# Kernel tuning notes

Hardware: AMD Instinct MI355X
Metric: run time of the kernel (lower is better)

The kernel has to match this reference:

```python
import jax, jax.numpy as jnp
import numpy as np

N, E, G = 100000, 400000, 2000   # nodes, edges, graphs
IN, H = 48, 128                  # in_channels, hidden_channels (= out_channels)
L = 6                            # num GIN layers
EPS = 1e-5                       # BatchNorm eps
SLOPE = 0.01                     # leaky_relu negative slope


def setup_inputs() -> dict:
    key = jax.random.key(0)
    ks = jax.random.split(key, 12)
    x = jax.random.normal(ks[0], (N, IN), jnp.float32)
    edge_index = jax.random.randint(ks[1], (2, E), 0, N)
    edge_attr = jax.random.normal(ks[2], (E, 4), jnp.float32)  # ignored by GINConv
    # sorted graph-assignment vector; guarantee every graph has >=1 node
    batch = jnp.sort(jnp.concatenate([jnp.arange(G),
                                      jax.random.randint(ks[3], (N - G,), 0, G)]))
    s = 0.05
    W1a = jax.random.normal(ks[4], (IN, H), jnp.float32) * s        # layer-0 MLP lin1
    W1b = jax.random.normal(ks[5], (L - 1, H, H), jnp.float32) * s  # layers 1..5 MLP lin1
    b1 = jnp.zeros((L, H), jnp.float32)
    g1 = jnp.ones((L, H), jnp.float32)    # inner BN scale
    be1 = jnp.zeros((L, H), jnp.float32)  # inner BN bias
    W2 = jax.random.normal(ks[6], (L, H, H), jnp.float32) * s       # MLP lin2
    b2 = jnp.zeros((L, H), jnp.float32)
    gn = jnp.ones((L - 1, H), jnp.float32)    # outer BN scale (layers 0..4)
    bn_b = jnp.zeros((L - 1, H), jnp.float32) # outer BN bias
    fc_w = jax.random.normal(ks[7], (2 * H, 64), jnp.float32) * s
    fc_b = jnp.zeros((64,), jnp.float32)
    fc2_w = jax.random.normal(ks[8], (64, 3), jnp.float32) * s
    fc2_b = jnp.zeros((3,), jnp.float32)
    return dict(x=x, edge_attr=edge_attr, W1a=W1a, W1b=W1b, b1=b1, g1=g1, be1=be1,
                W2=W2, b2=b2, gn=gn, bn_b=bn_b, fc_w=fc_w, fc_b=fc_b,
                fc2_w=fc2_w, fc2_b=fc2_b, edge_index=edge_index, batch=batch,
                num_graphs=G)


def _bn(h, g, b):
    # training-mode BatchNorm1d over node dim (biased variance, as torch)
    m = jnp.mean(h, axis=0)
    v = jnp.mean((h - m) ** 2, axis=0)
    return g * (h - m) * jax.lax.rsqrt(v + EPS) + b


def _lrelu(h):
    return jnp.where(h >= 0, h, SLOPE * h)


def reference(x, edge_attr, W1a, W1b, b1, g1, be1, W2, b2, gn, bn_b,
              fc_w, fc_b, fc2_w, fc2_b, edge_index, batch, num_graphs):
    del edge_attr  # GINConv does not use edge attributes
    src, dst = edge_index[0], edge_index[1]
    n = x.shape[0]
    h = x
    for l in range(L):
        # GINConv: (1 + eps) * x + sum_{j in N(i)} x_j, eps = 0
        agg = jax.ops.segment_sum(h[src], dst, num_segments=n)
        z = h + agg
        W1 = W1a if l == 0 else W1b[l - 1]
        # MLP([in, H, H]) with inner BatchNorm + leaky_relu, plain last linear
        z = _lrelu(_bn(z @ W1 + b1[l], g1[l], be1[l])) @ W2[l] + b2[l]
        if l < L - 1:  # outer norm + act, skipped on last layer
            z = _lrelu(_bn(z, gn[l], bn_b[l]))
        h = z
    # dual global pooling over ragged per-graph segments
    cnt = jax.ops.segment_sum(jnp.ones((n, 1), h.dtype), batch, num_segments=num_graphs)
    p1 = jax.ops.segment_sum(h, batch, num_segments=num_graphs) / jnp.maximum(cnt, 1.0)
    p2 = jax.ops.segment_max(h, batch, num_segments=num_graphs)
    emb = jnp.concatenate([p1, p2], axis=1)            # [G, 256]
    out = _lrelu(emb @ fc_w + fc_b) @ fc2_w + fc2_b    # [G, 3]
    return out, emb
```

## Files before the change

kernel.cpp:

```cpp
#include <hip/hip_runtime.h>
#include <stdint.h>

#define N_NODES 100000
#define N_EDGES 400000
#define N_GRAPHS 2000
#define C_IN 48
#define HD 128
#define NLAYERS 6
#define BN_EPS 1e-5f
#define NSLOPE 0.01f
#define SB 391
#define NREP 8
#define DBINS 33

typedef uint16_t u16;
typedef uint32_t u32;
typedef short bf16x8 __attribute__((ext_vector_type(8)));
typedef float f32x4 __attribute__((ext_vector_type(4)));

__device__ __forceinline__ float bf2f_lo(u32 v) { return __uint_as_float(v << 16); }
__device__ __forceinline__ float bf2f_hi(u32 v) { return __uint_as_float(v & 0xffff0000u); }
__device__ __forceinline__ float bf2f(u16 h) { return __uint_as_float(((u32)h) << 16); }
__device__ __forceinline__ u16 f2bf(float f) {
    u32 u = __float_as_uint(f);
    u32 r = (u + 0x7fffu + ((u >> 16) & 1u)) >> 16;
    return (u16)r;
}
__device__ __forceinline__ u32 pack2(float a, float b) {
    return (u32)f2bf(a) | ((u32)f2bf(b) << 16);
}
__device__ __forceinline__ float lrelu(float v) { return v >= 0.f ? v : v * NSLOPE; }

__device__ __forceinline__ void acc_bn(float* a, const uint4 v, const float* cA, const float* cB) {
    const u32 w[4] = {v.x, v.y, v.z, v.w};
    #pragma unroll
    for (int p = 0; p < 4; ++p) {
        a[2 * p]     += lrelu(cA[2 * p] * bf2f_lo(w[p]) + cB[2 * p]);
        a[2 * p + 1] += lrelu(cA[2 * p + 1] * bf2f_hi(w[p]) + cB[2 * p + 1]);
    }
}
__device__ __forceinline__ void acc_bf16row(float* a, const uint4 v) {
    const u32 w[4] = {v.x, v.y, v.z, v.w};
    #pragma unroll
    for (int p = 0; p < 4; ++p) {
        a[2 * p]     += bf2f_lo(w[p]);
        a[2 * p + 1] += bf2f_hi(w[p]);
    }
}
__device__ __forceinline__ void acc_f32row(float* a, const float* p) {
    const float4 u0 = reinterpret_cast<const float4*>(p)[0];
    const float4 u1 = reinterpret_cast<const float4*>(p)[1];
    a[0] += u0.x; a[1] += u0.y; a[2] += u0.z; a[3] += u0.w;
    a[4] += u1.x; a[5] += u1.y; a[6] += u1.z; a[7] += u1.w;
}

__global__ __launch_bounds__(256) void detect_kernel(const u16* __restrict__ x, int* __restrict__ mode) {
    __shared__ int flag;
    if (threadIdx.x == 0) flag = 0;
    __syncthreads();
    int local = 0;
    for (int i = threadIdx.x; i < 16384; i += 256) {
        float a = fabsf(bf2f(x[i]));
        if (!(a < 1e4f)) local = 1;
    }
    if (local) flag = 1;
    __syncthreads();
    if (threadIdx.x == 0) mode[0] = flag;
}

__global__ __launch_bounds__(256) void hist_kernel(const int* __restrict__ dst, int* __restrict__ cnt) {
    int e = blockIdx.x * 256 + threadIdx.x;
    if (e < N_EDGES) atomicAdd(&cnt[dst[e]], 1);
}

__global__ __launch_bounds__(256) void scan1_kernel(const int* __restrict__ cnt, int* __restrict__ bsum) {
    __shared__ int s[256];
    const int t = threadIdx.x;
    const int i = blockIdx.x * 256 + t;
    s[t] = (i < N_NODES) ? cnt[i] : 0;
    __syncthreads();
    for (int d = 128; d > 0; d >>= 1) {
        if (t < d) s[t] += s[t + d];
        __syncthreads();
    }
    if (t == 0) bsum[blockIdx.x] = s[0];
}

__global__ __launch_bounds__(512) void scan2_kernel(int* __restrict__ bsum, int* __restrict__ row_ptr) {
    __shared__ int s[SB];
    const int t = threadIdx.x;
    if (t < SB) s[t] = bsum[t];
    __syncthreads();
    if (t == 0) {
        int run = 0;
        for (int b = 0; b < SB; ++b) { int v = s[b]; s[b] = run; run += v; }
        row_ptr[0] = 0;
    }
    __syncthreads();
    if (t < SB) bsum[t] = s[t];
}

__global__ __launch_bounds__(256) void scan3_kernel(const int* __restrict__ cnt, const int* __restrict__ bsum,
                                                    int* __restrict__ row_ptr) {
    __shared__ int s[256];
    const int t = threadIdx.x;
    const int i = blockIdx.x * 256 + t;
    s[t] = (i < N_NODES) ? cnt[i] : 0;
    __syncthreads();
    if (t == 0) {
        int run = bsum[blockIdx.x];
        for (int j = 0; j < 256; ++j) { run += s[j]; s[j] = run; }
    }
    __syncthreads();
    if (i < N_NODES) row_ptr[i + 1] = s[t];
}

__global__ __launch_bounds__(256) void fill_kernel(const int* __restrict__ src, const int* __restrict__ dst,
                                                   int* __restrict__ cursor, int* __restrict__ col_idx) {
    int e = blockIdx.x * 256 + threadIdx.x;
    if (e < N_EDGES) {
        int d = dst[e];
        int slot = atomicAdd(&cursor[d], 1);
        col_idx[slot] = src[e];
    }
}

__global__ __launch_bounds__(256) void deg_hist_kernel(const int* __restrict__ row_ptr, int* __restrict__ dbins) {
    __shared__ int h[DBINS];
    const int tid = threadIdx.x;
    if (tid < DBINS) h[tid] = 0;
    __syncthreads();
    const int i = blockIdx.x * 256 + tid;
    if (i < N_NODES) atomicAdd(&h[min(row_ptr[i + 1] - row_ptr[i], 32)], 1);
    __syncthreads();
    if (tid < DBINS && h[tid]) atomicAdd(&dbins[tid], h[tid]);
}

__global__ __launch_bounds__(64) void deg_scan_kernel(int* __restrict__ dbins) {
    if (threadIdx.x == 0) {
        int run = 0;
        for (int b = 0; b < DBINS; ++b) { int v = dbins[b]; dbins[b] = run; run += v; }
    }
}

__global__ __launch_bounds__(256) void deg_scatter_kernel(const int* __restrict__ row_ptr, int* __restrict__ dbins,
                                                          int* __restrict__ perm) {
    __shared__ int cnt[DBINS];
    __shared__ int base[DBINS];
    const int tid = threadIdx.x;
    const int i = blockIdx.x * 256 + tid;
    if (tid < DBINS) cnt[tid] = 0;
    __syncthreads();
    int d = 0, local = 0;
    const bool act = i < N_NODES;
    if (act) {
        d = min(row_ptr[i + 1] - row_ptr[i], 32);
        local = atomicAdd(&cnt[d], 1);
    }
    __syncthreads();
    if (tid < DBINS) base[tid] = cnt[tid] ? atomicAdd(&dbins[tid], cnt[tid]) : 0;
    __syncthreads();
    if (act) perm[base[d] + local] = i;
}

__global__ __launch_bounds__(256) void pack_w_kernel(const void* __restrict__ W1a, const void* __restrict__ W1b,
                                                     const void* __restrict__ W2, const int* __restrict__ mode,
                                                     u16* __restrict__ wpack) {
    const int t = blockIdx.x * 256 + threadIdx.x;
    if (t >= 24576) return;
    const int mat = t >> 11;
    const int r = t & 2047;
    const int l = r & 63;
    const int f = r >> 6;
    const int kb = f >> 3, nt = f & 7;
    const int k0 = kb * 32 + (l >> 4) * 8;
    const int n = nt * 16 + (l & 15);
    const int md = *mode;
    u16 vals[8];
    #pragma unroll
    for (int j = 0; j < 8; ++j) {
        const int k = k0 + j;
        float v;
        if (mat == 0) {
            v = (k < C_IN) ? (md ? ((const float*)W1a)[k * HD + n] : bf2f(((const u16*)W1a)[k * HD + n])) : 0.f;
        } else if (mat < 6) {
            const size_t o = (size_t)(mat - 1) * HD * HD + (size_t)k * HD + n;
            v = md ? ((const float*)W1b)[o] : bf2f(((const u16*)W1b)[o]);
        } else {
            const size_t o = (size_t)(mat - 6) * HD * HD + (size_t)k * HD + n;
            v = md ? ((const float*)W2)[o] : bf2f(((const u16*)W2)[o]);
        }
        vals[j] = f2bf(v);
    }
    uint4 o;
    o.x = (u32)vals[0] | ((u32)vals[1] << 16);
    o.y = (u32)vals[2] | ((u32)vals[3] << 16);
    o.z = (u32)vals[4] | ((u32)vals[5] << 16);
    o.w = (u32)vals[6] | ((u32)vals[7] << 16);
    *reinterpret_cast<uint4*>(wpack + (size_t)t * 8) = o;
}

__global__ __launch_bounds__(256) void pack_b_kernel(const void* __restrict__ b1, const void* __restrict__ b2,
                                                     const int* __restrict__ mode, float* __restrict__ biasf) {
    const int i = blockIdx.x * 256 + threadIdx.x;
    if (i >= 12 * HD) return;
    const int mat = i >> 7, c = i & 127;
    const int md = *mode;
    float v;
    if (mat < 6) v = md ? ((const float*)b1)[mat * HD + c] : bf2f(((const u16*)b1)[mat * HD + c]);
    else         v = md ? ((const float*)b2)[(mat - 6) * HD + c] : bf2f(((const u16*)b2)[(mat - 6) * HD + c]);
    biasf[i] = v;
}

__device__ __forceinline__ void coef_to_lds(float* coefs, const float* __restrict__ instats,
                                            const void* __restrict__ gammav, const void* __restrict__ betav,
                                            size_t gelem, int md, int tid) {
    if (tid < 128) {
        float sm = 0.f, sq = 0.f;
        #pragma unroll
        for (int rep = 0; rep < NREP; ++rep) {
            sm += instats[rep * 256 + tid];
            sq += instats[rep * 256 + 128 + tid];
        }
        const float inv_n = 1.0f / (float)N_NODES;
        const float mean = sm * inv_n;
        const float var = fmaxf(sq * inv_n - mean * mean, 0.f);
        const float rs = rsqrtf(var + BN_EPS);
        const float g  = md ? ((const float*)gammav)[gelem + tid] : bf2f(((const u16*)gammav)[gelem + tid]);
        const float be = md ? ((const float*)betav)[gelem + tid]  : bf2f(((const u16*)betav)[gelem + tid]);
        const float A = g * rs;
        coefs[tid] = A;
        coefs[128 + tid] = be - A * mean;
    }
}

template <int TRANS, int STATS>
__global__ __launch_bounds__(256) void gemm_mfma(const u16* A, const u16* __restrict__ wp,
                                                 const float* __restrict__ biasf,
                                                 const float* __restrict__ instats,
                                                 const void* __restrict__ gammav, const void* __restrict__ betav,
                                                 size_t gelem, const int* __restrict__ mode,
                                                 u16* out, float* __restrict__ stats) {
    __shared__ u16 Asm[32][136];
    __shared__ float sred[2][128];
    __shared__ float sqred[2][128];
    __shared__ float coefs[256];
    const int tid = threadIdx.x;
    const int m0 = blockIdx.x * 32;
    const int rrow = tid >> 4;
    const int seg = tid & 15;

    if (TRANS) {
        coef_to_lds(coefs, instats, gammav, betav, gelem, *mode, tid);
        __syncthreads();
    }

    {
        float cA[8], cB[8];
        if (TRANS) {
            #pragma unroll
            for (int j = 0; j < 8; ++j) {
                cA[j] = coefs[seg * 8 + j];
                cB[j] = coefs[128 + seg * 8 + j];
            }
        }
        uint4 v[2];
        #pragma unroll
        for (int i = 0; i < 2; ++i) {
            const int gm = m0 + i * 16 + rrow;
            if (gm < N_NODES) v[i] = *reinterpret_cast<const uint4*>(A + (size_t)gm * HD + seg * 8);
            else { v[i].x = 0; v[i].y = 0; v[i].z = 0; v[i].w = 0; }
        }
        #pragma unroll
        for (int i = 0; i < 2; ++i) {
            uint4 o = v[i];
            if (TRANS) {
                u32 w[4] = {o.x, o.y, o.z, o.w};
                #pragma unroll
                for (int p = 0; p < 4; ++p) {
                    const float lo = lrelu(cA[2 * p] * bf2f_lo(w[p]) + cB[2 * p]);
                    const float hi = lrelu(cA[2 * p + 1] * bf2f_hi(w[p]) + cB[2 * p + 1]);
                    w[p] = pack2(lo, hi);
                }
                o.x = w[0]; o.y = w[1]; o.z = w[2]; o.w = w[3];
            }
            *reinterpret_cast<uint4*>(&Asm[i * 16 + rrow][seg * 8]) = o;
        }
    }
    __syncthreads();

    const int wave = tid >> 6, lane = tid & 63;
    const int quad = lane >> 4, lx = lane & 15;
    const int rowhalf = wave & 1;
    const int colhalf = wave >> 1;
    const int wrow = rowhalf * 16;
    f32x4 acc[4] = {};
    #pragma unroll
    for (int kb = 0; kb < 4; ++kb) {
        bf16x8 bfr[4];
        #pragma unroll
        for (int nt = 0; nt < 4; ++nt)
            bfr[nt] = *reinterpret_cast<const bf16x8*>(wp + (((size_t)(kb * 8 + colhalf * 4 + nt) * 64 + lane) << 3));
        const bf16x8 af = *reinterpret_cast<const bf16x8*>(&Asm[wrow + lx][kb * 32 + quad * 8]);
        #pragma unroll
        for (int nt = 0; nt < 4; ++nt)
            acc[nt] = __builtin_amdgcn_mfma_f32_16x16x32_bf16(af, bfr[nt], acc[nt], 0, 0, 0);
    }

    const int mrow0 = m0 + wrow;
    #pragma unroll
    for (int nt = 0; nt < 4; ++nt) {
        const int n = colhalf * 64 + nt * 16 + lx;
        const float bj = biasf[n];
        float s = 0.f, q = 0.f;
        #pragma unroll
        for (int r = 0; r < 4; ++r) {
            const int m = mrow0 + quad * 4 + r;
            if (m < N_NODES) {
                const float v = acc[nt][r] + bj;
                out[(size_t)m * HD + n] = f2bf(v);
                if (STATS) { s += v; q += v * v; }
            }
        }
        if (STATS) {
            s += __shfl_xor(s, 16); s += __shfl_xor(s, 32);
            q += __shfl_xor(q, 16); q += __shfl_xor(q, 32);
            if (quad == 0) { sred[rowhalf][n] = s; sqred[rowhalf][n] = q; }
        }
    }
    if (STATS) {
        __syncthreads();
        float* sdst = stats + (size_t)(blockIdx.x & (NREP - 1)) * 256;
        if (tid < 128) {
            atomicAdd(&sdst[tid], sred[0][tid] + sred[1][tid]);
        } else if (tid < 256) {
            const int c2 = tid - 128;
            atomicAdd(&sdst[128 + c2], sqred[0][c2] + sqred[1][c2]);
        }
    }
}

__global__ __launch_bounds__(256) void gemm_gather(const u16* __restrict__ U, const int* __restrict__ row_ptr,
                                                   const int* __restrict__ col_idx, const int* __restrict__ perm,
                                                   const u16* __restrict__ wp,
                                                   const float* __restrict__ biasf,
                                                   const float* __restrict__ instats,
                                                   const void* __restrict__ gammav, const void* __restrict__ betav,
                                                   size_t gelem, const int* __restrict__ mode,
                                                   u16* __restrict__ out, float* __restrict__ stats) {
    __shared__ u16 Asm[16][136];
    __shared__ float sred[128];
    __shared__ float sqred[128];
    __shared__ float coefs[256];
    __shared__ int sperm[16];
    const int tid = threadIdx.x;
    const int m0 = blockIdx.x * 16;
    const int rrow = tid >> 4;
    const int seg = tid & 15;

    coef_to_lds(coefs, instats, gammav, betav, gelem, *mode, tid);

    const int lm = m0 + rrow;
    int gm = -1;
    if (lm < N_NODES) gm = perm[lm];
    if (seg == 0) sperm[rrow] = gm;
    __syncthreads();

    {
        float cA[8], cB[8];
        #pragma unroll
        for (int j = 0; j < 8; ++j) {
            cA[j] = coefs[seg * 8 + j];
            cB[j] = coefs[128 + seg * 8 + j];
        }
        float a[8];
        #pragma unroll
        for (int j = 0; j < 8; ++j) a[j] = 0.f;
        if (gm >= 0) {
            const uint4 v = *reinterpret_cast<const uint4*>(U + (size_t)gm * HD + seg * 8);
            acc_bn(a, v, cA, cB);
            const int s = row_ptr[gm];
            const int deg = row_ptr[gm + 1] - s;
            int t = 0;
            for (; t + 4 <= deg; t += 4) {
                const int i0 = col_idx[s + t];
                const int i1 = col_idx[s + t + 1];
                const int i2 = col_idx[s + t + 2];
                const int i3 = col_idx[s + t + 3];
                const uint4 r0 = *reinterpret_cast<const uint4*>(U + (size_t)i0 * HD + seg * 8);
                const uint4 r1 = *reinterpret_cast<const uint4*>(U + (size_t)i1 * HD + seg * 8);
                const uint4 r2 = *reinterpret_cast<const uint4*>(U + (size_t)i2 * HD + seg * 8);
                const uint4 r3 = *reinterpret_cast<const uint4*>(U + (size_t)i3 * HD + seg * 8);
                acc_bn(a, r0, cA, cB);
                acc_bn(a, r1, cA, cB);
                acc_bn(a, r2, cA, cB);
                acc_bn(a, r3, cA, cB);
            }
            const int rem = deg - t;
            if (rem > 0) {
                const int i0 = col_idx[s + t];
                const uint4 r0 = *reinterpret_cast<const uint4*>(U + (size_t)i0 * HD + seg * 8);
                acc_bn(a, r0, cA, cB);
                if (rem > 1) {
                    const int i1 = col_idx[s + t + 1];
                    const uint4 r1 = *reinterpret_cast<const uint4*>(U + (size_t)i1 * HD + seg * 8);
                    acc_bn(a, r1, cA, cB);
                }
                if (rem > 2) {
                    const int i2 = col_idx[s + t + 2];
                    const uint4 r2 = *reinterpret_cast<const uint4*>(U + (size_t)i2 * HD + seg * 8);
                    acc_bn(a, r2, cA, cB);
                }
            }
        }
        uint4 o;
        o.x = pack2(a[0], a[1]); o.y = pack2(a[2], a[3]);
        o.z = pack2(a[4], a[5]); o.w = pack2(a[6], a[7]);
        *reinterpret_cast<uint4*>(&Asm[rrow][seg * 8]) = o;
    }
    __syncthreads();

    const int wave = tid >> 6, lane = tid & 63;
    const int quad = lane >> 4, lx = lane & 15;
    f32x4 acc[2] = {};
    #pragma unroll
    for (int kb = 0; kb < 4; ++kb) {
        bf16x8 bfr[2];
        #pragma unroll
        for (int nt = 0; nt < 2; ++nt)
            bfr[nt] = *reinterpret_cast<const bf16x8*>(wp + (((size_t)(kb * 8 + wave * 2 + nt) * 64 + lane) << 3));
        const bf16x8 af = *reinterpret_cast<const bf16x8*>(&Asm[lx][kb * 32 + quad * 8]);
        #pragma unroll
        for (int nt = 0; nt < 2; ++nt)
            acc[nt] = __builtin_amdgcn_mfma_f32_16x16x32_bf16(af, bfr[nt], acc[nt], 0, 0, 0);
    }

    #pragma unroll
    for (int nt = 0; nt < 2; ++nt) {
        const int n = wave * 32 + nt * 16 + lx;
        const float bj = biasf[n];
        float s = 0.f, q = 0.f;
        #pragma unroll
        for (int r = 0; r < 4; ++r) {
            const int lr = m0 + quad * 4 + r;
            if (lr < N_NODES) {
                const int m = sperm[quad * 4 + r];
                const float v = acc[nt][r] + bj;
                out[(size_t)m * HD + n] = f2bf(v);
                s += v; q += v * v;
            }
        }
        s += __shfl_xor(s, 16); s += __shfl_xor(s, 32);
        q += __shfl_xor(q, 16); q += __shfl_xor(q, 32);
        if (quad == 0) { sred[n] = s; sqred[n] = q; }
    }
    __syncthreads();
    float* sdst = stats + (size_t)(blockIdx.x & (NREP - 1)) * 256;
    if (tid < 128) {
        atomicAdd(&sdst[tid], sred[tid]);
    } else if (tid < 256) {
        const int c2 = tid - 128;
        atomicAdd(&sdst[128 + c2], sqred[c2]);
    }
}

__global__ __launch_bounds__(256) void gemm_gather0(const void* __restrict__ xv, const int* __restrict__ row_ptr,
                                                    const int* __restrict__ col_idx, const int* __restrict__ perm,
                                                    const u16* __restrict__ wp,
                                                    const float* __restrict__ biasf, const int* __restrict__ mode,
                                                    u16* __restrict__ out, float* __restrict__ stats) {
    __shared__ u16 Asm[16][136];
    __shared__ float sred[128];
    __shared__ float sqred[128];
    __shared__ int sperm[16];
    const int tid = threadIdx.x;
    const int m0 = blockIdx.x * 16;
    const int rrow = tid >> 4;
    const int seg = tid & 15;
    const int md = *mode;
    const bool act = seg < 6;

    const int lm = m0 + rrow;
    int gm = -1;
    if (lm < N_NODES) gm = perm[lm];
    if (seg == 0) sperm[rrow] = gm;

    {
        float a[8];
        #pragma unroll
        for (int j = 0; j < 8; ++j) a[j] = 0.f;
        if (gm >= 0 && act) {
            if (md) {
                acc_f32row(a, (const float*)xv + (size_t)gm * C_IN + seg * 8);
            } else {
                acc_bf16row(a, *reinterpret_cast<const uint4*>((const u16*)xv + (size_t)gm * C_IN + seg * 8));
            }
            const int s = row_ptr[gm];
            const int deg = row_ptr[gm + 1] - s;
            int t = 0;
            for (; t + 4 <= deg; t += 4) {
                const int i0 = col_idx[s + t];
                const int i1 = col_idx[s + t + 1];
                const int i2 = col_idx[s + t + 2];
                const int i3 = col_idx[s + t + 3];
                if (md) {
                    acc_f32row(a, (const float*)xv + (size_t)i0 * C_IN + seg * 8);
                    acc_f32row(a, (const float*)xv + (size_t)i1 * C_IN + seg * 8);
                    acc_f32row(a, (const float*)xv + (size_t)i2 * C_IN + seg * 8);
                    acc_f32row(a, (const float*)xv + (size_t)i3 * C_IN + seg * 8);
                } else {
                    acc_bf16row(a, *reinterpret_cast<const uint4*>((const u16*)xv + (size_t)i0 * C_IN + seg * 8));
                    acc_bf16row(a, *reinterpret_cast<const uint4*>((const u16*)xv + (size_t)i1 * C_IN + seg * 8));
                    acc_bf16row(a, *reinterpret_cast<const uint4*>((const u16*)xv + (size_t)i2 * C_IN + seg * 8));
                    acc_bf16row(a, *reinterpret_cast<const uint4*>((const u16*)xv + (size_t)i3 * C_IN + seg * 8));
                }
            }
            const int rem = deg - t;
            if (rem > 0) {
                const int i0 = col_idx[s + t];
                if (md) acc_f32row(a, (const float*)xv + (size_t)i0 * C_IN + seg * 8);
                else    acc_bf16row(a, *reinterpret_cast<const uint4*>((const u16*)xv + (size_t)i0 * C_IN + seg * 8));
                if (rem > 1) {
                    const int i1 = col_idx[s + t + 1];
                    if (md) acc_f32row(a, (const float*)xv + (size_t)i1 * C_IN + seg * 8);
                    else    acc_bf16row(a, *reinterpret_cast<const uint4*>((const u16*)xv + (size_t)i1 * C_IN + seg * 8));
                }
                if (rem > 2) {
                    const int i2 = col_idx[s + t + 2];
                    if (md) acc_f32row(a, (const float*)xv + (size_t)i2 * C_IN + seg * 8);
                    else    acc_bf16row(a, *reinterpret_cast<const uint4*>((const u16*)xv + (size_t)i2 * C_IN + seg * 8));
                }
            }
        }
        uint4 o;
        o.x = pack2(a[0], a[1]); o.y = pack2(a[2], a[3]);
        o.z = pack2(a[4], a[5]); o.w = pack2(a[6], a[7]);
        *reinterpret_cast<uint4*>(&Asm[rrow][seg * 8]) = o;
    }
    __syncthreads();

    const int wave = tid >> 6, lane = tid & 63;
    const int quad = lane >> 4, lx = lane & 15;
    f32x4 acc[2] = {};
    #pragma unroll
    for (int kb = 0; kb < 4; ++kb) {
        bf16x8 bfr[2];
        #pragma unroll
        for (int nt = 0; nt < 2; ++nt)
            bfr[nt] = *reinterpret_cast<const bf16x8*>(wp + (((size_t)(kb * 8 + wave * 2 + nt) * 64 + lane) << 3));
        const bf16x8 af = *reinterpret_cast<const bf16x8*>(&Asm[lx][kb * 32 + quad * 8]);
        #pragma unroll
        for (int nt = 0; nt < 2; ++nt)
            acc[nt] = __builtin_amdgcn_mfma_f32_16x16x32_bf16(af, bfr[nt], acc[nt], 0, 0, 0);
    }

    #pragma unroll
    for (int nt = 0; nt < 2; ++nt) {
        const int n = wave * 32 + nt * 16 + lx;
        const float bj = biasf[n];
        float s = 0.f, q = 0.f;
        #pragma unroll
        for (int r = 0; r < 4; ++r) {
            const int lr = m0 + quad * 4 + r;
            if (lr < N_NODES) {
                const int m = sperm[quad * 4 + r];
                const float v = acc[nt][r] + bj;
                out[(size_t)m * HD + n] = f2bf(v);
                s += v; q += v * v;
            }
        }
        s += __shfl_xor(s, 16); s += __shfl_xor(s, 32);
        q += __shfl_xor(q, 16); q += __shfl_xor(q, 32);
        if (quad == 0) { sred[n] = s; sqred[n] = q; }
    }
    __syncthreads();
    float* sdst = stats + (size_t)(blockIdx.x & (NREP - 1)) * 256;
    if (tid < 128) {
        atomicAdd(&sdst[tid], sred[tid]);
    } else if (tid < 256) {
        const int c2 = tid - 128;
        atomicAdd(&sdst[128 + c2], sqred[c2]);
    }
}

__global__ __launch_bounds__(256) void pool_kernel(const u16* __restrict__ hf, const int* __restrict__ batch,
                                                   const int* __restrict__ mode, float* __restrict__ emb,
                                                   void* __restrict__ outv) {
    const int wave = threadIdx.x >> 6, lane = threadIdx.x & 63;
    const int g = blockIdx.x * 4 + wave;
    if (g >= N_GRAPHS) return;
    const int md = *mode;
    const int quad = lane >> 4, c = lane & 15;
    int lo = 0, hi = N_NODES;
    while (lo < hi) { int m = (lo + hi) >> 1; if (batch[m] < g) lo = m + 1; else hi = m; }
    const int s = lo;
    hi = N_NODES;
    while (lo < hi) { int m = (lo + hi) >> 1; if (batch[m] < g + 1) lo = m + 1; else hi = m; }
    const int e = lo;
    const int cnt = e - s;
    float sum[8], mx[8];
    #pragma unroll
    for (int j = 0; j < 8; ++j) { sum[j] = 0.f; mx[j] = -INFINITY; }
    for (int n = s + quad; n < e; n += 4) {
        const uint4 v = *reinterpret_cast<const uint4*>(hf + (size_t)n * HD + c * 8);
        const u32 w[4] = {v.x, v.y, v.z, v.w};
        #pragma unroll
        for (int p = 0; p < 4; ++p) {
            const float f0 = bf2f_lo(w[p]), f1 = bf2f_hi(w[p]);
            sum[2 * p] += f0; sum[2 * p + 1] += f1;
            mx[2 * p] = fmaxf(mx[2 * p], f0); mx[2 * p + 1] = fmaxf(mx[2 * p + 1], f1);
        }
    }
    #pragma unroll
    for (int j = 0; j < 8; ++j) {
        sum[j] += __shfl_xor(sum[j], 16); sum[j] += __shfl_xor(sum[j], 32);
        mx[j] = fmaxf(mx[j], __shfl_xor(mx[j], 16));
        mx[j] = fmaxf(mx[j], __shfl_xor(mx[j], 32));
    }
    if (quad == 0) {
        const float invc = 1.0f / (float)max(cnt, 1);
        const size_t base = (size_t)N_GRAPHS * 3 + (size_t)g * 256;
        #pragma unroll
        for (int j = 0; j < 8; ++j) {
            const float mean = sum[j] * invc;
            const float m2 = (cnt == 0) ? 0.f : mx[j];
            const int col = c * 8 + j;
            emb[(size_t)g * 256 + col] = mean;
            emb[(size_t)g * 256 + 128 + col] = m2;
            if (md) {
                ((float*)outv)[base + col] = mean;
                ((float*)outv)[base + 128 + col] = m2;
            } else {
                ((u16*)outv)[base + col] = f2bf(mean);
                ((u16*)outv)[base + 128 + col] = f2bf(m2);
            }
        }
    }
}

__global__ __launch_bounds__(64) void final_kernel(const float* __restrict__ emb, const void* __restrict__ fcwv,
                                                   const void* __restrict__ fcbv, const void* __restrict__ fc2wv,
                                                   const void* __restrict__ fc2bv, const int* __restrict__ mode,
                                                   void* __restrict__ outv) {
    __shared__ float es[256];
    __shared__ float hs[64];
    const int g = blockIdx.x, t = threadIdx.x;
    const int md = *mode;
    reinterpret_cast<float4*>(es)[t] = reinterpret_cast<const float4*>(emb + (size_t)g * 256)[t];
    __syncthreads();
    float acc = md ? ((const float*)fcbv)[t] : bf2f(((const u16*)fcbv)[t]);
    if (md) {
        const float* w = (const float*)fcwv;
        #pragma unroll 8
        for (int k = 0; k < 256; ++k) acc += es[k] * w[k * 64 + t];
    } else {
        const u16* w = (const u16*)fcwv;
        #pragma unroll 8
        for (int k = 0; k < 256; ++k) acc += es[k] * bf2f(w[k * 64 + t]);
    }
    hs[t] = lrelu(acc);
    __syncthreads();
    if (t < 3) {
        float o = md ? ((const float*)fc2bv)[t] : bf2f(((const u16*)fc2bv)[t]);
        if (md) {
            const float* w = (const float*)fc2wv;
            #pragma unroll 8
            for (int j = 0; j < 64; ++j) o += hs[j] * w[j * 3 + t];
            ((float*)outv)[(size_t)g * 3 + t] = o;
        } else {
            const u16* w = (const u16*)fc2wv;
            #pragma unroll 8
            for (int j = 0; j < 64; ++j) o += hs[j] * bf2f(w[j * 3 + t]);
            ((u16*)outv)[(size_t)g * 3 + t] = f2bf(o);
        }
    }
}

static inline size_t align256(size_t x) { return (x + 255) & ~(size_t)255; }

extern "C" void kernel_launch(void* const* d_in, const int* in_sizes, int n_in,
                              void* d_out, int out_size, void* d_ws, size_t ws_size,
                              hipStream_t stream) {
    (void)in_sizes; (void)n_in; (void)out_size; (void)ws_size;
    const void* x    = d_in[0];
    const void* W1a  = d_in[2];
    const void* W1b  = d_in[3];
    const void* b1   = d_in[4];
    const void* g1   = d_in[5];
    const void* be1  = d_in[6];
    const void* W2   = d_in[7];
    const void* b2   = d_in[8];
    const void* gn   = d_in[9];
    const void* bnb  = d_in[10];
    const void* fcw  = d_in[11];
    const void* fcb  = d_in[12];
    const void* fc2w = d_in[13];
    const void* fc2b = d_in[14];
    const int* ei    = (const int*)d_in[15];
    const int* batch = (const int*)d_in[16];

    char* p = (char*)d_ws;
    size_t off = 0;
    u16* zb = (u16*)(p + off); off += align256((size_t)N_NODES * HD * 2);
    u16* hb = (u16*)(p + off); off += align256((size_t)N_NODES * HD * 2);
    u16* wpack = (u16*)(p + off); off += align256((size_t)12 * HD * HD * 2);
    float* biasf = (float*)(p + off); off += align256((size_t)12 * HD * 4);
    float* emb = (float*)(p + off); off += align256((size_t)N_GRAPHS * 256 * 4);
    int* row_ptr = (int*)(p + off); off += align256((size_t)(N_NODES + 1) * 4);
    int* cursor = (int*)(p + off); off += align256((size_t)N_NODES * 4);
    int* col_idx = (int*)(p + off); off += align256((size_t)N_EDGES * 4);
    int* bsum = (int*)(p + off); off += align256((size_t)SB * 4);
    float* statsAll = (float*)(p + off); off += align256((size_t)12 * NREP * 256 * 4);
    int* perm = (int*)(p + off); off += align256((size_t)N_NODES * 4);
    int* dbins = (int*)(p + off); off += align256((size_t)64 * 4);
    int* mode = (int*)(p + off); off += align256(4);

    const int EB = (N_EDGES + 255) / 256;
    const int GBM = (N_NODES + 31) / 32;
    const int GBG = (N_NODES + 15) / 16;

    detect_kernel<<<1, 256, 0, stream>>>((const u16*)x, mode);

    hipMemsetAsync(cursor, 0, (size_t)N_NODES * 4, stream);
    hipMemsetAsync(statsAll, 0, (size_t)12 * NREP * 256 * 4, stream);
    hipMemsetAsync(dbins, 0, (size_t)DBINS * 4, stream);
    hist_kernel<<<EB, 256, 0, stream>>>(ei + N_EDGES, cursor);
    scan1_kernel<<<SB, 256, 0, stream>>>(cursor, bsum);
    scan2_kernel<<<1, 512, 0, stream>>>(bsum, row_ptr);
    scan3_kernel<<<SB, 256, 0, stream>>>(cursor, bsum, row_ptr);
    deg_hist_kernel<<<SB, 256, 0, stream>>>(row_ptr, dbins);
    deg_scan_kernel<<<1, 64, 0, stream>>>(dbins);
    deg_scatter_kernel<<<SB, 256, 0, stream>>>(row_ptr, dbins, perm);
    hipMemcpyAsync(cursor, row_ptr, (size_t)N_NODES * 4, hipMemcpyDeviceToDevice, stream);
    fill_kernel<<<EB, 256, 0, stream>>>(ei, ei + N_EDGES, cursor, col_idx);
    pack_w_kernel<<<96, 256, 0, stream>>>(W1a, W1b, W2, mode, wpack);
    pack_b_kernel<<<6, 256, 0, stream>>>(b1, b2, mode, biasf);

    u16* cur = zb;
    u16* oth = hb;
    for (int l = 0; l < NLAYERS; ++l) {
        float* statsA = statsAll + (size_t)l * NREP * 256;
        float* statsB = statsAll + (size_t)(6 + l) * NREP * 256;
        float* statsBprev = statsAll + (size_t)(6 + l - 1) * NREP * 256;
        if (l == 0) {
            gemm_gather0<<<GBG, 256, 0, stream>>>(x, row_ptr, col_idx, perm, wpack,
                                                  biasf, mode, cur, statsA);
        } else {
            gemm_gather<<<GBG, 256, 0, stream>>>(cur, row_ptr, col_idx, perm,
                                                 wpack + (size_t)l * HD * HD,
                                                 biasf + (size_t)l * HD, statsBprev, gn, bnb,
                                                 (size_t)(l - 1) * HD, mode, oth, statsA);
            u16* t = cur; cur = oth; oth = t;
        }
        if (l < NLAYERS - 1) {
            gemm_mfma<1, 1><<<GBM, 256, 0, stream>>>(cur, wpack + (size_t)(6 + l) * HD * HD,
                                                     biasf + (size_t)(6 + l) * HD, statsA, g1, be1,
                                                     (size_t)l * HD, mode, cur, statsB);
        } else {
            gemm_mfma<1, 0><<<GBM, 256, 0, stream>>>(cur, wpack + (size_t)(6 + l) * HD * HD,
                                                     biasf + (size_t)(6 + l) * HD, statsA, g1, be1,
                                                     (size_t)l * HD, mode, cur, nullptr);
        }
    }

    pool_kernel<<<(N_GRAPHS + 3) / 4, 256, 0, stream>>>(cur, batch, mode, emb, d_out);
    final_kernel<<<N_GRAPHS, 64, 0, stream>>>(emb, fcw, fcb, fc2w, fc2b, mode, d_out);
}
```

Baseline: 526.7 us.

## Store node features in degree-sorted order and gather two rows per thread

Node features are now kept in permuted (degree-sorted, descending) order, so the gather/GEMM kernels write their outputs contiguously and read the self row directly. col_idx is remapped through an inverse permutation, and pooling looks rows up via pos. The gather kernels now handle 32 rows per block, two rows per thread with an interleaved neighbor loop, so more loads are in flight. This drops the scattered output writes, but pooling now reads rows indirectly and bounds checks are removed because N is a multiple of 32.

```diff
diff --git a/kernel.cpp b/kernel.cpp
--- a/kernel.cpp
+++ b/kernel.cpp
@@ -53,6 +53,10 @@
     a[0] += u0.x; a[1] += u0.y; a[2] += u0.z; a[3] += u0.w;
     a[4] += u1.x; a[5] += u1.y; a[6] += u1.z; a[7] += u1.w;
 }
+__device__ __forceinline__ void ld_xrow(float* a, const void* xv, int md, int idx, int seg) {
+    if (md) acc_f32row(a, (const float*)xv + (size_t)idx * C_IN + seg * 8);
+    else    acc_bf16row(a, *reinterpret_cast<const uint4*>((const u16*)xv + (size_t)idx * C_IN + seg * 8));
+}
 
 __global__ __launch_bounds__(256) void detect_kernel(const u16* __restrict__ x, int* __restrict__ mode) {
     __shared__ int flag;
@@ -116,12 +120,13 @@
 }
 
 __global__ __launch_bounds__(256) void fill_kernel(const int* __restrict__ src, const int* __restrict__ dst,
+                                                   const int* __restrict__ pos,
                                                    int* __restrict__ cursor, int* __restrict__ col_idx) {
     int e = blockIdx.x * 256 + threadIdx.x;
     if (e < N_EDGES) {
         int d = dst[e];
         int slot = atomicAdd(&cursor[d], 1);
-        col_idx[slot] = src[e];
+        col_idx[slot] = pos[src[e]];
     }
 }
 
@@ -139,7 +144,7 @@
 __global__ __launch_bounds__(64) void deg_scan_kernel(int* __restrict__ dbins) {
     if (threadIdx.x == 0) {
         int run = 0;
-        for (int b = 0; b < DBINS; ++b) { int v = dbins[b]; dbins[b] = run; run += v; }
+        for (int b = DBINS - 1; b >= 0; --b) { int v = dbins[b]; dbins[b] = run; run += v; }
     }
 }
 
@@ -161,6 +166,11 @@
     if (tid < DBINS) base[tid] = cnt[tid] ? atomicAdd(&dbins[tid], cnt[tid]) : 0;
     __syncthreads();
     if (act) perm[base[d] + local] = i;
+}
+
+__global__ __launch_bounds__(256) void inv_kernel(const int* __restrict__ perm, int* __restrict__ pos) {
+    const int i = blockIdx.x * 256 + threadIdx.x;
+    if (i < N_NODES) pos[perm[i]] = i;
 }
 
 __global__ __launch_bounds__(256) void pack_w_kernel(const void* __restrict__ W1a, const void* __restrict__ W1b,
@@ -341,29 +351,23 @@
 }
 
 __global__ __launch_bounds__(256) void gemm_gather(const u16* __restrict__ U, const int* __restrict__ row_ptr,
-                                                   const int* __restrict__ col_idx, const int* __restrict__ perm,
+                                                   const int* __restrict__ col2, const int* __restrict__ perm,
                                                    const u16* __restrict__ wp,
                                                    const float* __restrict__ biasf,
                                                    const float* __restrict__ instats,
                                                    const void* __restrict__ gammav, const void* __restrict__ betav,
                                                    size_t gelem, const int* __restrict__ mode,
                                                    u16* __restrict__ out, float* __restrict__ stats) {
-    __shared__ u16 Asm[16][136];
-    __shared__ float sred[128];
-    __shared__ float sqred[128];
+    __shared__ u16 Asm[32][136];
+    __shared__ float sred[2][128];
+    __shared__ float sqred[2][128];
     __shared__ float coefs[256];
-    __shared__ int sperm[16];
     const int tid = threadIdx.x;
-    const int m0 = blockIdx.x * 16;
+    const int m0 = blockIdx.x * 32;
     const int rrow = tid >> 4;
     const int seg = tid & 15;
 
     coef_to_lds(coefs, instats, gammav, betav, gelem, *mode, tid);
-
-    const int lm = m0 + rrow;
-    int gm = -1;
-    if (lm < N_NODES) gm = perm[lm];
-    if (seg == 0) sperm[rrow] = gm;
     __syncthreads();
 
     {
@@ -373,217 +377,193 @@
             cA[j] = coefs[seg * 8 + j];
             cB[j] = coefs[128 + seg * 8 + j];
         }
-        float a[8];
-        #pragma unroll
-        for (int j = 0; j < 8; ++j) a[j] = 0.f;
-        if (gm >= 0) {
-            const uint4 v = *reinterpret_cast<const uint4*>(U + (size_t)gm * HD + seg * 8);
-            acc_bn(a, v, cA, cB);
-            const int s = row_ptr[gm];
-            const int deg = row_ptr[gm + 1] - s;
-            int t = 0;
-            for (; t + 4 <= deg; t += 4) {
-                const int i0 = col_idx[s + t];
-                const int i1 = col_idx[s + t + 1];
-                const int i2 = col_idx[s + t + 2];
-                const int i3 = col_idx[s + t + 3];
-                const uint4 r0 = *reinterpret_cast<const uint4*>(U + (size_t)i0 * HD + seg * 8);
-                const uint4 r1 = *reinterpret_cast<const uint4*>(U + (size_t)i1 * HD + seg * 8);
-                const uint4 r2 = *reinterpret_cast<const uint4*>(U + (size_t)i2 * HD + seg * 8);
-                const uint4 r3 = *reinterpret_cast<const uint4*>(U + (size_t)i3 * HD + seg * 8);
-                acc_bn(a, r0, cA, cB);
-                acc_bn(a, r1, cA, cB);
-                acc_bn(a, r2, cA, cB);
-                acc_bn(a, r3, cA, cB);
-            }
-            const int rem = deg - t;
-            if (rem > 0) {
-                const int i0 = col_idx[s + t];
-                const uint4 r0 = *reinterpret_cast<const uint4*>(U + (size_t)i0 * HD + seg * 8);
-                acc_bn(a, r0, cA, cB);
-                if (rem > 1) {
-                    const int i1 = col_idx[s + t + 1];
-                    const uint4 r1 = *reinterpret_cast<const uint4*>(U + (size_t)i1 * HD + seg * 8);
-                    acc_bn(a, r1, cA, cB);
-                }
-                if (rem > 2) {
-                    const int i2 = col_idx[s + t + 2];
-                    const uint4 r2 = *reinterpret_cast<const uint4*>(U + (size_t)i2 * HD + seg * 8);
-                    acc_bn(a, r2, cA, cB);
-                }
-            }
-        }
-        uint4 o;
-        o.x = pack2(a[0], a[1]); o.y = pack2(a[2], a[3]);
-        o.z = pack2(a[4], a[5]); o.w = pack2(a[6], a[7]);
-        *reinterpret_cast<uint4*>(&Asm[rrow][seg * 8]) = o;
+        const int lm0 = m0 + rrow;
+        const int lm1 = m0 + 16 + rrow;
+        const int gm0 = perm[lm0];
+        const int gm1 = perm[lm1];
+        float a0[8], a1[8];
+        #pragma unroll
+        for (int j = 0; j < 8; ++j) { a0[j] = 0.f; a1[j] = 0.f; }
+        const uint4 v0 = *reinterpret_cast<const uint4*>(U + (size_t)lm0 * HD + seg * 8);
+        const uint4 v1 = *reinterpret_cast<const uint4*>(U + (size_t)lm1 * HD + seg * 8);
+        acc_bn(a0, v0, cA, cB);
+        acc_bn(a1, v1, cA, cB);
+        const int s0 = row_ptr[gm0], d0 = row_ptr[gm0 + 1] - s0;
+        const int s1 = row_ptr[gm1], d1 = row_ptr[gm1 + 1] - s1;
+        const int dm = max(d0, d1);
+        for (int t = 0; t < dm; t += 2) {
+            const bool p00 = t < d0, p01 = (t + 1) < d0;
+            const bool p10 = t < d1, p11 = (t + 1) < d1;
+            int i00 = 0, i01 = 0, i10 = 0, i11 = 0;
+            if (p00) i00 = col2[s0 + t];
+            if (p01) i01 = col2[s0 + t + 1];
+            if (p10) i10 = col2[s1 + t];
+            if (p11) i11 = col2[s1 + t + 1];
+            uint4 r00{}, r01{}, r10{}, r11{};
+            if (p00) r00 = *reinterpret_cast<const uint4*>(U + (size_t)i00 * HD + seg * 8);
+            if (p01) r01 = *reinterpret_cast<const uint4*>(U + (size_t)i01 * HD + seg * 8);
+            if (p10) r10 = *reinterpret_cast<const uint4*>(U + (size_t)i10 * HD + seg * 8);
+            if (p11) r11 = *reinterpret_cast<const uint4*>(U + (size_t)i11 * HD + seg * 8);
+            if (p00) acc_bn(a0, r00, cA, cB);
+            if (p01) acc_bn(a0, r01, cA, cB);
+            if (p10) acc_bn(a1, r10, cA, cB);
+            if (p11) acc_bn(a1, r11, cA, cB);
+        }
+        uint4 o0, o1;
+        o0.x = pack2(a0[0], a0[1]); o0.y = pack2(a0[2], a0[3]);
+        o0.z = pack2(a0[4], a0[5]); o0.w = pack2(a0[6], a0[7]);
+        o1.x = pack2(a1[0], a1[1]); o1.y = pack2(a1[2], a1[3]);
+        o1.z = pack2(a1[4], a1[5]); o1.w = pack2(a1[6], a1[7]);
+        *reinterpret_cast<uint4*>(&Asm[rrow][seg * 8]) = o0;
+        *reinterpret_cast<uint4*>(&Asm[16 + rrow][seg * 8]) = o1;
     }
     __syncthreads();
 
     const int wave = tid >> 6, lane = tid & 63;
     const int quad = lane >> 4, lx = lane & 15;
-    f32x4 acc[2] = {};
+    const int rowhalf = wave & 1;
+    const int colhalf = wave >> 1;
+    const int wrow = rowhalf * 16;
+    f32x4 acc[4] = {};
     #pragma unroll
     for (int kb = 0; kb < 4; ++kb) {
-        bf16x8 bfr[2];
-        #pragma unroll
-        for (int nt = 0; nt < 2; ++nt)
-            bfr[nt] = *reinterpret_cast<const bf16x8*>(wp + (((size_t)(kb * 8 + wave * 2 + nt) * 64 + lane) << 3));
-        const bf16x8 af = *reinterpret_cast<const bf16x8*>(&Asm[lx][kb * 32 + quad * 8]);
-        #pragma unroll
-        for (int nt = 0; nt < 2; ++nt)
+        bf16x8 bfr[4];
+        #pragma unroll
+        for (int nt = 0; nt < 4; ++nt)
+            bfr[nt] = *reinterpret_cast<const bf16x8*>(wp + (((size_t)(kb * 8 + colhalf * 4 + nt) * 64 + lane) << 3));
+        const bf16x8 af = *reinterpret_cast<const bf16x8*>(&Asm[wrow + lx][kb * 32 + quad * 8]);
+        #pragma unroll
+        for (int nt = 0; nt < 4; ++nt)
             acc[nt] = __builtin_amdgcn_mfma_f32_16x16x32_bf16(af, bfr[nt], acc[nt], 0, 0, 0);
     }
 
-    #pragma unroll
-    for (int nt = 0; nt < 2; ++nt) {
-        const int n = wave * 32 + nt * 16 + lx;
+    const int mrow0 = m0 + wrow;
+    #pragma unroll
+    for (int nt = 0; nt < 4; ++nt) {
+        const int n = colhalf * 64 + nt * 16 + lx;
         const float bj = biasf[n];
         float s = 0.f, q = 0.f;
         #pragma unroll
         for (int r = 0; r < 4; ++r) {
-            const int lr = m0 + quad * 4 + r;
-            if (lr < N_NODES) {
-                const int m = sperm[quad * 4 + r];
-                const float v = acc[nt][r] + bj;
-                out[(size_t)m * HD + n] = f2bf(v);
-                s += v; q += v * v;
-            }
+            const int m = mrow0 + quad * 4 + r;
+            const float v = acc[nt][r] + bj;
+            out[(size_t)m * HD + n] = f2bf(v);
+            s += v; q += v * v;
         }
         s += __shfl_xor(s, 16); s += __shfl_xor(s, 32);
         q += __shfl_xor(q, 16); q += __shfl_xor(q, 32);
-        if (quad == 0) { sred[n] = s; sqred[n] = q; }
+        if (quad == 0) { sred[rowhalf][n] = s; sqred[rowhalf][n] = q; }
     }
     __syncthreads();
     float* sdst = stats + (size_t)(blockIdx.x & (NREP - 1)) * 256;
     if (tid < 128) {
-        atomicAdd(&sdst[tid], sred[tid]);
+        atomicAdd(&sdst[tid], sred[0][tid] + sred[1][tid]);
     } else if (tid < 256) {
         const int c2 = tid - 128;
-        atomicAdd(&sdst[128 + c2], sqred[c2]);
+        atomicAdd(&sdst[128 + c2], sqred[0][c2] + sqred[1][c2]);
     }
 }
 
 __global__ __launch_bounds__(256) void gemm_gather0(const void* __restrict__ xv, const int* __restrict__ row_ptr,
-                                                    const int* __restrict__ col_idx, const int* __restrict__ perm,
+                                                    const int* __restrict__ col2, const int* __restrict__ perm,
                                                     const u16* __restrict__ wp,
                                                     const float* __restrict__ biasf, const int* __restrict__ mode,
                                                     u16* __restrict__ out, float* __restrict__ stats) {
-    __shared__ u16 Asm[16][136];
-    __shared__ float sred[128];
-    __shared__ float sqred[128];
-    __shared__ int sperm[16];
+    __shared__ u16 Asm[32][136];
+    __shared__ float sred[2][128];
+    __shared__ float sqred[2][128];
     const int tid = threadIdx.x;
-    const int m0 = blockIdx.x * 16;
+    const int m0 = blockIdx.x * 32;
     const int rrow = tid >> 4;
     const int seg = tid & 15;
     const int md = *mode;
     const bool act = seg < 6;
 
-    const int lm = m0 + rrow;
-    int gm = -1;
-    if (lm < N_NODES) gm = perm[lm];
-    if (seg == 0) sperm[rrow] = gm;
-
     {
-        float a[8];
-        #pragma unroll
-        for (int j = 0; j < 8; ++j) a[j] = 0.f;
-        if (gm >= 0 && act) {
-            if (md) {
-                acc_f32row(a, (const float*)xv + (size_t)gm * C_IN + seg * 8);
-            } else {
-                acc_bf16row(a, *reinterpret_cast<const uint4*>((const u16*)xv + (size_t)gm * C_IN + seg * 8));
+        const int lm0 = m0 + rrow;
+        const int lm1 = m0 + 16 + rrow;
+        const int gm0 = perm[lm0];
+        const int gm1 = perm[lm1];
+        float a0[8], a1[8];
+        #pragma unroll
+        for (int j = 0; j < 8; ++j) { a0[j] = 0.f; a1[j] = 0.f; }
+        const int s0 = row_ptr[gm0], d0 = row_ptr[gm0 + 1] - s0;
+        const int s1 = row_ptr[gm1], d1 = row_ptr[gm1 + 1] - s1;
+        if (act) {
+            ld_xrow(a0, xv, md, gm0, seg);
+            ld_xrow(a1, xv, md, gm1, seg);
+            const int dm = max(d0, d1);
+            for (int t = 0; t < dm; t += 2) {
+                const bool p00 = t < d0, p01 = (t + 1) < d0;
+                const bool p10 = t < d1, p11 = (t + 1) < d1;
+                int i00 = 0, i01 = 0, i10 = 0, i11 = 0;
+                if (p00) i00 = perm[col2[s0 + t]];
+                if (p01) i01 = perm[col2[s0 + t + 1]];
+                if (p10) i10 = perm[col2[s1 + t]];
+                if (p11) i11 = perm[col2[s1 + t + 1]];
+                if (p00) ld_xrow(a0, xv, md, i00, seg);
+                if (p01) ld_xrow(a0, xv, md, i01, seg);
+                if (p10) ld_xrow(a1, xv, md, i10, seg);
+                if (p11) ld_xrow(a1, xv, md, i11, seg);
             }
-            const int s = row_ptr[gm];
-            const int deg = row_ptr[gm + 1] - s;
-            int t = 0;
-            for (; t + 4 <= deg; t += 4) {
-                const int i0 = col_idx[s + t];
-                const int i1 = col_idx[s + t + 1];
-                const int i2 = col_idx[s + t + 2];
-                const int i3 = col_idx[s + t + 3];
-                if (md) {
-                    acc_f32row(a, (const float*)xv + (size_t)i0 * C_IN + seg * 8);
-                    acc_f32row(a, (const float*)xv + (size_t)i1 * C_IN + seg * 8);
-                    acc_f32row(a, (const float*)xv + (size_t)i2 * C_IN + seg * 8);
-                    acc_f32row(a, (const float*)xv + (size_t)i3 * C_IN + seg * 8);
-                } else {
-                    acc_bf16row(a, *reinterpret_cast<const uint4*>((const u16*)xv + (size_t)i0 * C_IN + seg * 8));
-                    acc_bf16row(a, *reinterpret_cast<const uint4*>((const u16*)xv + (size_t)i1 * C_IN + seg * 8));
-                    acc_bf16row(a, *reinterpret_cast<const uint4*>((const u16*)xv + (size_t)i2 * C_IN + seg * 8));
-                    acc_bf16row(a, *reinterpret_cast<const uint4*>((const u16*)xv + (size_t)i3 * C_IN + seg * 8));
-                }
-            }
-            const int rem = deg - t;
-            if (rem > 0) {
-                const int i0 = col_idx[s + t];
-                if (md) acc_f32row(a, (const float*)xv + (size_t)i0 * C_IN + seg * 8);
-                else    acc_bf16row(a, *reinterpret_cast<const uint4*>((const u16*)xv + (size_t)i0 * C_IN + seg * 8));
-                if (rem > 1) {
-                    const int i1 = col_idx[s + t + 1];
-                    if (md) acc_f32row(a, (const float*)xv + (size_t)i1 * C_IN + seg * 8);
-                    else    acc_bf16row(a, *reinterpret_cast<const uint4*>((const u16*)xv + (size_t)i1 * C_IN + seg * 8));
-                }
-                if (rem > 2) {
-                    const int i2 = col_idx[s + t + 2];
-                    if (md) acc_f32row(a, (const float*)xv + (size_t)i2 * C_IN + seg * 8);
-                    else    acc_bf16row(a, *reinterpret_cast<const uint4*>((const u16*)xv + (size_t)i2 * C_IN + seg * 8));
-                }
-            }
-        }
-        uint4 o;
-        o.x = pack2(a[0], a[1]); o.y = pack2(a[2], a[3]);
-        o.z = pack2(a[4], a[5]); o.w = pack2(a[6], a[7]);
-        *reinterpret_cast<uint4*>(&Asm[rrow][seg * 8]) = o;
+        }
+        uint4 o0, o1;
+        o0.x = pack2(a0[0], a0[1]); o0.y = pack2(a0[2], a0[3]);
+        o0.z = pack2(a0[4], a0[5]); o0.w = pack2(a0[6], a0[7]);
+        o1.x = pack2(a1[0], a1[1]); o1.y = pack2(a1[2], a1[3]);
+        o1.z = pack2(a1[4], a1[5]); o1.w = pack2(a1[6], a1[7]);
+        *reinterpret_cast<uint4*>(&Asm[rrow][seg * 8]) = o0;
+        *reinterpret_cast<uint4*>(&Asm[16 + rrow][seg * 8]) = o1;
     }
     __syncthreads();
 
     const int wave = tid >> 6, lane = tid & 63;
     const int quad = lane >> 4, lx = lane & 15;
-    f32x4 acc[2] = {};
+    const int rowhalf = wave & 1;
+    const int colhalf = wave >> 1;
+    const int wrow = rowhalf * 16;
+    f32x4 acc[4] = {};
     #pragma unroll
     for (int kb = 0; kb < 4; ++kb) {
-        bf16x8 bfr[2];
-        #pragma unroll
-        for (int nt = 0; nt < 2; ++nt)
-            bfr[nt] = *reinterpret_cast<const bf16x8*>(wp + (((size_t)(kb * 8 + wave * 2 + nt) * 64 + lane) << 3));
-        const bf16x8 af = *reinterpret_cast<const bf16x8*>(&Asm[lx][kb * 32 + quad * 8]);
-        #pragma unroll
-        for (int nt = 0; nt < 2; ++nt)
+        bf16x8 bfr[4];
+        #pragma unroll
+        for (int nt = 0; nt < 4; ++nt)
+            bfr[nt] = *reinterpret_cast<const bf16x8*>(wp + (((size_t)(kb * 8 + colhalf * 4 + nt) * 64 + lane) << 3));
+        const bf16x8 af = *reinterpret_cast<const bf16x8*>(&Asm[wrow + lx][kb * 32 + quad * 8]);
+        #pragma unroll
+        for (int nt = 0; nt < 4; ++nt)
             acc[nt] = __builtin_amdgcn_mfma_f32_16x16x32_bf16(af, bfr[nt], acc[nt], 0, 0, 0);
     }
 
-    #pragma unroll
-    for (int nt = 0; nt < 2; ++nt) {
-        const int n = wave * 32 + nt * 16 + lx;
+    const int mrow0 = m0 + wrow;
+    #pragma unroll
+    for (int nt = 0; nt < 4; ++nt) {
+        const int n = colhalf * 64 + nt * 16 + lx;
         const float bj = biasf[n];
         float s = 0.f, q = 0.f;
         #pragma unroll
         for (int r = 0; r < 4; ++r) {
-            const int lr = m0 + quad * 4 + r;
-            if (lr < N_NODES) {
-                const int m = sperm[quad * 4 + r];
-                const float v = acc[nt][r] + bj;
-                out[(size_t)m * HD + n] = f2bf(v);
-                s += v; q += v * v;
-            }
+            const int m = mrow0 + quad * 4 + r;
+            const float v = acc[nt][r] + bj;
+            out[(size_t)m * HD + n] = f2bf(v);
+            s += v; q += v * v;
         }
         s += __shfl_xor(s, 16); s += __shfl_xor(s, 32);
         q += __shfl_xor(q, 16); q += __shfl_xor(q, 32);
-        if (quad == 0) { sred[n] = s; sqred[n] = q; }
+        if (quad == 0) { sred[rowhalf][n] = s; sqred[rowhalf][n] = q; }
     }
     __syncthreads();
     float* sdst = stats + (size_t)(blockIdx.x & (NREP - 1)) * 256;
     if (tid < 128) {
-        atomicAdd(&sdst[tid], sred[tid]);
+        atomicAdd(&sdst[tid], sred[0][tid] + sred[1][tid]);
     } else if (tid < 256) {
         const int c2 = tid - 128;
-        atomicAdd(&sdst[128 + c2], sqred[c2]);
+        atomicAdd(&sdst[128 + c2], sqred[0][c2] + sqred[1][c2]);
     }
 }
 
 __global__ __launch_bounds__(256) void pool_kernel(const u16* __restrict__ hf, const int* __restrict__ batch,
+                                                   const int* __restrict__ pos,
                                                    const int* __restrict__ mode, float* __restrict__ emb,
                                                    void* __restrict__ outv) {
     const int wave = threadIdx.x >> 6, lane = threadIdx.x & 63;
@@ -602,13 +582,14 @@
     #pragma unroll
     for (int j = 0; j < 8; ++j) { sum[j] = 0.f; mx[j] = -INFINITY; }
     for (int n = s + quad; n < e; n += 4) {
-        const uint4 v = *reinterpret_cast<const uint4*>(hf + (size_t)n * HD + c * 8);
+        const int p = pos[n];
+        const uint4 v = *reinterpret_cast<const uint4*>(hf + (size_t)p * HD + c * 8);
         const u32 w[4] = {v.x, v.y, v.z, v.w};
         #pragma unroll
-        for (int p = 0; p < 4; ++p) {
-            const float f0 = bf2f_lo(w[p]), f1 = bf2f_hi(w[p]);
-            sum[2 * p] += f0; sum[2 * p + 1] += f1;
-            mx[2 * p] = fmaxf(mx[2 * p], f0); mx[2 * p + 1] = fmaxf(mx[2 * p + 1], f1);
+        for (int pp = 0; pp < 4; ++pp) {
+            const float f0 = bf2f_lo(w[pp]), f1 = bf2f_hi(w[pp]);
+            sum[2 * pp] += f0; sum[2 * pp + 1] += f1;
+            mx[2 * pp] = fmaxf(mx[2 * pp], f0); mx[2 * pp + 1] = fmaxf(mx[2 * pp + 1], f1);
         }
     }
     #pragma unroll
@@ -712,12 +693,12 @@
     int* bsum = (int*)(p + off); off += align256((size_t)SB * 4);
     float* statsAll = (float*)(p + off); off += align256((size_t)12 * NREP * 256 * 4);
     int* perm = (int*)(p + off); off += align256((size_t)N_NODES * 4);
+    int* pos = (int*)(p + off); off += align256((size_t)N_NODES * 4);
     int* dbins = (int*)(p + off); off += align256((size_t)64 * 4);
     int* mode = (int*)(p + off); off += align256(4);
 
     const int EB = (N_EDGES + 255) / 256;
-    const int GBM = (N_NODES + 31) / 32;
-    const int GBG = (N_NODES + 15) / 16;
+    const int GB32 = N_NODES / 32;
 
     detect_kernel<<<1, 256, 0, stream>>>((const u16*)x, mode);
 
@@ -731,8 +712,9 @@
     deg_hist_kernel<<<SB, 256, 0, stream>>>(row_ptr, dbins);
     deg_scan_kernel<<<1, 64, 0, stream>>>(dbins);
     deg_scatter_kernel<<<SB, 256, 0, stream>>>(row_ptr, dbins, perm);
+    inv_kernel<<<SB, 256, 0, stream>>>(perm, pos);
     hipMemcpyAsync(cursor, row_ptr, (size_t)N_NODES * 4, hipMemcpyDeviceToDevice, stream);
-    fill_kernel<<<EB, 256, 0, stream>>>(ei, ei + N_EDGES, cursor, col_idx);
+    fill_kernel<<<EB, 256, 0, stream>>>(ei, ei + N_EDGES, pos, cursor, col_idx);
     pack_w_kernel<<<96, 256, 0, stream>>>(W1a, W1b, W2, mode, wpack);
     pack_b_kernel<<<6, 256, 0, stream>>>(b1, b2, mode, biasf);
 
@@ -743,26 +725,26 @@
         float* statsB = statsAll + (size_t)(6 + l) * NREP * 256;
         float* statsBprev = statsAll + (size_t)(6 + l - 1) * NREP * 256;
         if (l == 0) {
-            gemm_gather0<<<GBG, 256, 0, stream>>>(x, row_ptr, col_idx, perm, wpack,
-                                                  biasf, mode, cur, statsA);
+            gemm_gather0<<<GB32, 256, 0, stream>>>(x, row_ptr, col_idx, perm, wpack,
+                                                   biasf, mode, cur, statsA);
         } else {
-            gemm_gather<<<GBG, 256, 0, stream>>>(cur, row_ptr, col_idx, perm,
-                                                 wpack + (size_t)l * HD * HD,
-                                                 biasf + (size_t)l * HD, statsBprev, gn, bnb,
-                                                 (size_t)(l - 1) * HD, mode, oth, statsA);
+            gemm_gather<<<GB32, 256, 0, stream>>>(cur, row_ptr, col_idx, perm,
+                                                  wpack + (size_t)l * HD * HD,
+                                                  biasf + (size_t)l * HD, statsBprev, gn, bnb,
+                                                  (size_t)(l - 1) * HD, mode, oth, statsA);
             u16* t = cur; cur = oth; oth = t;
         }
         if (l < NLAYERS - 1) {
-            gemm_mfma<1, 1><<<GBM, 256, 0, stream>>>(cur, wpack + (size_t)(6 + l) * HD * HD,
-                                                     biasf + (size_t)(6 + l) * HD, statsA, g1, be1,
-                                                     (size_t)l * HD, mode, cur, statsB);
+            gemm_mfma<1, 1><<<GB32, 256, 0, stream>>>(cur, wpack + (size_t)(6 + l) * HD * HD,
+                                                      biasf + (size_t)(6 + l) * HD, statsA, g1, be1,
+                                                      (size_t)l * HD, mode, cur, statsB);
         } else {
-            gemm_mfma<1, 0><<<GBM, 256, 0, stream>>>(cur, wpack + (size_t)(6 + l) * HD * HD,
-                                                     biasf + (size_t)(6 + l) * HD, statsA, g1, be1,
-                                                     (size_t)l * HD, mode, cur, nullptr);
-        }
-    }
-
-    pool_kernel<<<(N_GRAPHS + 3) / 4, 256, 0, stream>>>(cur, batch, mode, emb, d_out);
+            gemm_mfma<1, 0><<<GB32, 256, 0, stream>>>(cur, wpack + (size_t)(6 + l) * HD * HD,
+                                                      biasf + (size_t)(6 + l) * HD, statsA, g1, be1,
+                                                      (size_t)l * HD, mode, cur, nullptr);
+        }
+    }
+
+    pool_kernel<<<(N_GRAPHS + 3) / 4, 256, 0, stream>>>(cur, batch, pos, mode, emb, d_out);
     final_kernel<<<N_GRAPHS, 64, 0, stream>>>(emb, fcw, fcb, fc2w, fc2b, mode, d_out);
 }
```

Result: faster. 494.7 us (-6.1%).
